# Optimization experiments

Hardware: AMD Instinct MI355X
Metric: run time of the kernel (lower is better)

Reference implementation:

```python
import jax, jax.numpy as jnp
import numpy as np

B, S, D = 4, 2048, 1024
E = 4          # moe_capacity
K = 2          # top-k experts
F = 4 * D      # expert hidden width


def setup_inputs() -> dict:
    key = jax.random.key(0)
    ks = jax.random.split(key, 8)
    scale_in = 1.0 / np.sqrt(D)
    scale_hid = 1.0 / np.sqrt(F)
    return {
        "x": jax.random.normal(ks[0], (B, S, D), dtype=jnp.float32),
        "Wg": jax.random.normal(ks[1], (D, E), dtype=jnp.float32) * scale_in,
        "bg": jnp.zeros((E,), dtype=jnp.float32),
        "W1": jax.random.normal(ks[2], (E, D, F), dtype=jnp.float32) * scale_in,
        "b1": jnp.zeros((E, F), dtype=jnp.float32),
        "W2": jax.random.normal(ks[3], (E, F, D), dtype=jnp.float32) * scale_hid,
        "b2": jnp.zeros((E, D), dtype=jnp.float32),
    }


def reference(x, Wg, bg, W1, b1, W2, b2):
    # Gating: top-k expert indices per token (scores are NOT used as weights
    # in the original module; the combine mask is a binary one-hot sum).
    gate_logits = jnp.einsum("bsd,de->bse", x, Wg) + bg          # [B,S,E]
    _, idx = jax.lax.top_k(gate_logits, K)                        # [B,S,K]
    mask = jnp.sum(jax.nn.one_hot(idx, E, dtype=x.dtype), axis=-2)  # [B,S,E], 0/1

    # All-experts dense compute (faithful to original wasteful fallback).
    h = jax.nn.swish(jnp.einsum("bsd,edf->bsef", x, W1) + b1)     # [B,S,E,F]
    y = jnp.einsum("bsef,efd->bsed", h, W2) + b2                  # [B,S,E,D]

    # Mask-and-sum combine over experts.
    out = jnp.einsum("bsed,bse->bsd", y, mask)                    # [B,S,D]
    return out.astype(jnp.float32)
```

## Files before the change

### kernel.cpp

```cpp
#include <hip/hip_runtime.h>
#include <hip/hip_fp16.h>

#define D_DIM 1024
#define E_NUM 4
#define F_DIM 4096
#define NTOK 8192
#define MT 64
#define FC 256
#define KC 256
#define FHALF 2048
#define NWORK 520
#define NWORK_A 4160
#define NWORK_B 2080
#define HROWS_MAX 16640

typedef _Float16 half8_t __attribute__((ext_vector_type(8)));
typedef _Float16 half4_t __attribute__((ext_vector_type(4)));
typedef float floatx4 __attribute__((ext_vector_type(4)));

template<bool WRITE_XH>
__global__ __launch_bounds__(256) void gate_kernel(
    const float* __restrict__ x, const float* __restrict__ Wg,
    const float* __restrict__ bg, _Float16* __restrict__ xh,
    int* __restrict__ cnt, int* __restrict__ lists)
{
    __shared__ int sel[32];
    __shared__ int loc[4][32];
    __shared__ int lbase[4], lnum[4];

    int wave = threadIdx.x >> 6;
    int lane = threadIdx.x & 63;
    int tbase = blockIdx.x * 32;

    for (int i = 0; i < 8; ++i) {
        int slot = wave * 8 + i;
        int tok = tbase + slot;
        const float* xr = x + (size_t)tok * D_DIM;
        double a0 = 0.0, a1 = 0.0, a2 = 0.0, a3 = 0.0;
        #pragma unroll
        for (int it = 0; it < 4; ++it) {
            int i0 = it * 256 + lane * 4;
            float4 xv = *(const float4*)(xr + i0);
            if (WRITE_XH) {
                half4_t hv = { (_Float16)xv.x, (_Float16)xv.y,
                               (_Float16)xv.z, (_Float16)xv.w };
                *(half4_t*)(xh + (size_t)tok * D_DIM + i0) = hv;
            }
            float4 w0 = *(const float4*)(Wg + (size_t)i0 * 4);
            float4 w1 = *(const float4*)(Wg + (size_t)i0 * 4 + 4);
            float4 w2 = *(const float4*)(Wg + (size_t)i0 * 4 + 8);
            float4 w3 = *(const float4*)(Wg + (size_t)i0 * 4 + 12);
            a0 += (double)xv.x * w0.x + (double)xv.y * w1.x
                + (double)xv.z * w2.x + (double)xv.w * w3.x;
            a1 += (double)xv.x * w0.y + (double)xv.y * w1.y
                + (double)xv.z * w2.y + (double)xv.w * w3.y;
            a2 += (double)xv.x * w0.z + (double)xv.y * w1.z
                + (double)xv.z * w2.z + (double)xv.w * w3.z;
            a3 += (double)xv.x * w0.w + (double)xv.y * w1.w
                + (double)xv.z * w2.w + (double)xv.w * w3.w;
        }
        #pragma unroll
        for (int off = 32; off > 0; off >>= 1) {
            a0 += __shfl_down(a0, off);
            a1 += __shfl_down(a1, off);
            a2 += __shfl_down(a2, off);
            a3 += __shfl_down(a3, off);
        }
        if (lane == 0) {
            double lg[4] = { a0 + (double)bg[0], a1 + (double)bg[1],
                             a2 + (double)bg[2], a3 + (double)bg[3] };
            int i1 = 0;
            for (int e = 1; e < 4; ++e) if (lg[e] > lg[i1]) i1 = e;
            int i2 = -1;
            for (int e = 0; e < 4; ++e) {
                if (e == i1) continue;
                if (i2 < 0 || lg[e] > lg[i2]) i2 = e;
            }
            sel[slot] = i1 * 4 + i2;
        }
    }
    __syncthreads();
    if (threadIdx.x < 4) {
        int e = threadIdx.x, n = 0;
        for (int s = 0; s < 32; ++s) {
            int v = sel[s];
            if ((v >> 2) == e || (v & 3) == e) loc[e][n++] = tbase + s;
        }
        lnum[e] = n;
        lbase[e] = atomicAdd(&cnt[e], n);
    }
    __syncthreads();
    {
        int e = threadIdx.x >> 6;
        int j = threadIdx.x & 63;
        if (j < lnum[e]) lists[e * NTOK + lbase[e] + j] = loc[e][j];
    }
}

__global__ __launch_bounds__(256) void tile_pack_kernel(
    const float* __restrict__ src, _Float16* __restrict__ dst, int R, int C)
{
    __shared__ _Float16 t2[32][36];
    int r0 = blockIdx.y * 32, c0 = blockIdx.x * 32;
    const float* s = src + (size_t)blockIdx.z * R * C;
    _Float16* d = dst + (size_t)blockIdx.z * R * C;
    int tx = threadIdx.x & 31, ty = threadIdx.x >> 5;
    #pragma unroll
    for (int i = 0; i < 4; ++i) {
        int r = ty + i * 8;
        t2[tx][r] = (_Float16)s[(size_t)(r0 + r) * C + c0 + tx];
    }
    __syncthreads();
    int KB = R >> 5;
    int idx = threadIdx.x * 4;
    int frag_h = idx >> 9;
    int rem = idx & 511;
    int quad = rem >> 7, ln = (rem >> 3) & 15, j0 = rem & 7;
    int cl = frag_h * 16 + ln, rl = quad * 8 + j0;
    half4_t v = { t2[cl][rl], t2[cl][rl + 1], t2[cl][rl + 2], t2[cl][rl + 3] };
    size_t off = ((size_t)(((c0 >> 4) + frag_h) * KB + (r0 >> 5))) * 512 + rem;
    *(half4_t*)&d[off] = v;
}

__device__ __forceinline__ void decode_tile(
    int r, int nb0, int nb1, int nb2,
    int& expert, int& tile, int& hbase)
{
    if (r < nb0)                  { expert = 0; tile = r;                 hbase = 0; }
    else if (r < nb0 + nb1)       { expert = 1; tile = r - nb0;           hbase = nb0; }
    else if (r < nb0 + nb1 + nb2) { expert = 2; tile = r - nb0 - nb1;     hbase = nb0 + nb1; }
    else                          { expert = 3; tile = r - nb0 - nb1 - nb2; hbase = nb0 + nb1 + nb2; }
}

__global__ __launch_bounds__(512, 4) void h1_kernel(
    const _Float16* __restrict__ xh, const _Float16* __restrict__ W1m,
    const float* __restrict__ b1, const int* __restrict__ cnt,
    const int* __restrict__ lists, _Float16* __restrict__ Hbuf)
{
    __shared__ _Float16 Xs[MT][KC + 8];
    __shared__ _Float16 Hsd[MT][FC + 8];
    __shared__ int tks[MT];

    int b = blockIdx.x;
    int work = (b & 7) * (NWORK_A / 8) + (b >> 3);

    int nb0 = (cnt[0] + MT - 1) / MT;
    int nb1 = (cnt[1] + MT - 1) / MT;
    int nb2 = (cnt[2] + MT - 1) / MT;
    int nb3 = (cnt[3] + MT - 1) / MT;
    int T = nb0 + nb1 + nb2 + nb3;
    if (work >= 16 * T) return;

    int fc = work / T;
    int r  = work % T;
    int expert, tile, hbase;
    decode_tile(r, nb0, nb1, nb2, expert, tile, hbase);
    int mcnt = min(MT, cnt[expert] - tile * MT);

    if (threadIdx.x < MT) {
        int idx = tile * MT + (int)threadIdx.x;
        tks[threadIdx.x] = lists[expert * NTOK + ((int)threadIdx.x < mcnt ? idx : tile * MT)];
    }
    __syncthreads();

    const half8_t* W1f = (const half8_t*)(W1m + (size_t)expert * D_DIM * F_DIM);
    const float* b1e = b1 + (size_t)expert * F_DIM;

    int w = threadIdx.x >> 6;
    int lane = threadIdx.x & 63;
    int quad = lane >> 4;
    int ln = lane & 15;
    int srow = threadIdx.x >> 3;
    int stg  = threadIdx.x & 7;

    int f0 = fc * FC;
    int fb0 = (f0 >> 4) + w * 2;

    floatx4 hacc[4][2];
    #pragma unroll
    for (int mt = 0; mt < 4; ++mt) { hacc[mt][0] = (floatx4){0.f,0.f,0.f,0.f};
                                     hacc[mt][1] = (floatx4){0.f,0.f,0.f,0.f}; }

    for (int kc = 0; kc < D_DIM / KC; ++kc) {
        int k0 = kc * KC;
        {
            const _Float16* xr = xh + (size_t)tks[srow] * D_DIM + k0 + stg * 32;
            half8_t v0 = *(const half8_t*)(xr);
            half8_t v1 = *(const half8_t*)(xr + 8);
            half8_t v2 = *(const half8_t*)(xr + 16);
            half8_t v3 = *(const half8_t*)(xr + 24);
            *(half8_t*)&Xs[srow][stg * 32]      = v0;
            *(half8_t*)&Xs[srow][stg * 32 + 8]  = v1;
            *(half8_t*)&Xs[srow][stg * 32 + 16] = v2;
            *(half8_t*)&Xs[srow][stg * 32 + 24] = v3;
        }
        __syncthreads();

        #pragma unroll
        for (int ks = 0; ks < KC / 32; ++ks) {
            int kk = ks * 32 + quad * 8;
            int kb = kc * 8 + ks;
            half8_t a[4];
            #pragma unroll
            for (int mt = 0; mt < 4; ++mt)
                a[mt] = *(const half8_t*)&Xs[mt * 16 + ln][kk];
            #pragma unroll
            for (int nt = 0; nt < 2; ++nt) {
                half8_t bfr = W1f[((size_t)((fb0 + nt) * 32 + kb)) * 64 + lane];
                #pragma unroll
                for (int mt = 0; mt < 4; ++mt)
                    hacc[mt][nt] = __builtin_amdgcn_mfma_f32_16x16x32_f16(
                        a[mt], bfr, hacc[mt][nt], 0, 0, 0);
            }
        }
        __syncthreads();
    }

    #pragma unroll
    for (int nt = 0; nt < 2; ++nt) {
        int fcol_l = w * 32 + nt * 16 + ln;
        float b1v = b1e[f0 + fcol_l];
        #pragma unroll
        for (int mt = 0; mt < 4; ++mt)
            #pragma unroll
            for (int r2 = 0; r2 < 4; ++r2) {
                float v = hacc[mt][nt][r2] + b1v;
                float hs = v / (1.f + __expf(-v));
                Hsd[mt * 16 + quad * 4 + r2][fcol_l] = (_Float16)hs;
            }
    }
    __syncthreads();

    {
        size_t hrow0 = ((size_t)(hbase + tile)) * MT;
        _Float16* hdst = Hbuf + (hrow0 + srow) * F_DIM + f0 + stg * 32;
        const _Float16* hsrc = &Hsd[srow][stg * 32];
        half8_t v0 = *(const half8_t*)(hsrc);
        half8_t v1 = *(const half8_t*)(hsrc + 8);
        half8_t v2 = *(const half8_t*)(hsrc + 16);
        half8_t v3 = *(const half8_t*)(hsrc + 24);
        *(half8_t*)(hdst)      = v0;
        *(half8_t*)(hdst + 8)  = v1;
        *(half8_t*)(hdst + 16) = v2;
        *(half8_t*)(hdst + 24) = v3;
    }
}

__global__ __launch_bounds__(512, 4) void o2_kernel(
    const _Float16* __restrict__ Hbuf, const _Float16* __restrict__ W2m,
    const float* __restrict__ b2, const int* __restrict__ cnt,
    const int* __restrict__ lists, float* __restrict__ out)
{
    __shared__ _Float16 Hs[MT][KC + 8];
    __shared__ int tks[MT];

    int b = blockIdx.x;
    int work = (b & 7) * (NWORK_B / 8) + (b >> 3);

    int nb0 = (cnt[0] + MT - 1) / MT;
    int nb1 = (cnt[1] + MT - 1) / MT;
    int nb2 = (cnt[2] + MT - 1) / MT;
    int nb3 = (cnt[3] + MT - 1) / MT;
    int T = nb0 + nb1 + nb2 + nb3;
    if (work >= 8 * T) return;

    int s = work / T;
    int r = work % T;
    int dq = s >> 1;
    int kh = s & 1;
    int expert, tile, hbase;
    decode_tile(r, nb0, nb1, nb2, expert, tile, hbase);
    int mcnt = min(MT, cnt[expert] - tile * MT);

    if (threadIdx.x < MT) {
        int idx = tile * MT + (int)threadIdx.x;
        tks[threadIdx.x] = lists[expert * NTOK + ((int)threadIdx.x < mcnt ? idx : tile * MT)];
    }
    __syncthreads();

    const half8_t* W2f = (const half8_t*)(W2m + (size_t)expert * D_DIM * F_DIM);
    const float* b2e = b2 + (size_t)expert * D_DIM;

    int w = threadIdx.x >> 6;
    int lane = threadIdx.x & 63;
    int quad = lane >> 4;
    int ln = lane & 15;
    int srow = threadIdx.x >> 3;
    int stg  = threadIdx.x & 7;

    size_t hrow0 = ((size_t)(hbase + tile)) * MT;
    const _Float16* hrow = Hbuf + (hrow0 + srow) * F_DIM + stg * 32;

    floatx4 oacc[4][2];
    #pragma unroll
    for (int mt = 0; mt < 4; ++mt) { oacc[mt][0] = (floatx4){0.f,0.f,0.f,0.f};
                                     oacc[mt][1] = (floatx4){0.f,0.f,0.f,0.f}; }

    for (int kc = kh * 8; kc < kh * 8 + 8; ++kc) {
        {
            const _Float16* hr = hrow + kc * KC;
            half8_t v0 = *(const half8_t*)(hr);
            half8_t v1 = *(const half8_t*)(hr + 8);
            half8_t v2 = *(const half8_t*)(hr + 16);
            half8_t v3 = *(const half8_t*)(hr + 24);
            *(half8_t*)&Hs[srow][stg * 32]      = v0;
            *(half8_t*)&Hs[srow][stg * 32 + 8]  = v1;
            *(half8_t*)&Hs[srow][stg * 32 + 16] = v2;
            *(half8_t*)&Hs[srow][stg * 32 + 24] = v3;
        }
        __syncthreads();

        #pragma unroll
        for (int ks = 0; ks < KC / 32; ++ks) {
            int kk = ks * 32 + quad * 8;
            int fkb = kc * 8 + ks;
            half8_t a[4];
            #pragma unroll
            for (int mt = 0; mt < 4; ++mt)
                a[mt] = *(const half8_t*)&Hs[mt * 16 + ln][kk];
            #pragma unroll
            for (int nt = 0; nt < 2; ++nt) {
                int db = dq * 16 + w * 2 + nt;
                half8_t bfr = W2f[((size_t)(db * 128 + fkb)) * 64 + lane];
                #pragma unroll
                for (int mt = 0; mt < 4; ++mt)
                    oacc[mt][nt] = __builtin_amdgcn_mfma_f32_16x16x32_f16(
                        a[mt], bfr, oacc[mt][nt], 0, 0, 0);
            }
        }
        __syncthreads();
    }

    #pragma unroll
    for (int mt = 0; mt < 4; ++mt) {
        #pragma unroll
        for (int r2 = 0; r2 < 4; ++r2) {
            int row = mt * 16 + quad * 4 + r2;
            if (row >= mcnt) continue;
            float* orow = out + (size_t)tks[row] * D_DIM;
            #pragma unroll
            for (int nt = 0; nt < 2; ++nt) {
                int dcol = dq * 256 + w * 32 + nt * 16 + ln;
                float v = oacc[mt][nt][r2];
                if (kh == 0) v += b2e[dcol];
                atomicAdd(orow + dcol, v);
            }
        }
    }
}

__global__ __launch_bounds__(512, 2) void moe_fast_kernel(
    const _Float16* __restrict__ xh, const _Float16* __restrict__ W1m,
    const float* __restrict__ b1, const _Float16* __restrict__ W2m,
    const float* __restrict__ b2, const int* __restrict__ cnt,
    const int* __restrict__ lists, float* __restrict__ out)
{
    __shared__ _Float16 Xs[MT][KC + 8];
    __shared__ _Float16 Hsd[MT][FC + 8];
    __shared__ int tks[MT];

    int b = blockIdx.x;
    int work = (b & 7) * (NWORK / 8) + (b >> 3);

    int nb0 = (cnt[0] + MT - 1) / MT;
    int nb1 = (cnt[1] + MT - 1) / MT;
    int nb2 = (cnt[2] + MT - 1) / MT;
    int nb3 = (cnt[3] + MT - 1) / MT;
    int T = nb0 + nb1 + nb2 + nb3;

    int fhalf, r;
    if (work < T) { fhalf = 0; r = work; }
    else if (work < 2 * T) { fhalf = 1; r = work - T; }
    else return;

    int expert, tile, hbase;
    decode_tile(r, nb0, nb1, nb2, expert, tile, hbase);
    int mcnt = min(MT, cnt[expert] - tile * MT);

    if (threadIdx.x < MT) {
        int idx = tile * MT + (int)threadIdx.x;
        tks[threadIdx.x] = lists[expert * NTOK + ((int)threadIdx.x < mcnt ? idx : tile * MT)];
    }
    __syncthreads();

    const half8_t* W1f = (const half8_t*)(W1m + (size_t)expert * D_DIM * F_DIM);
    const half8_t* W2f = (const half8_t*)(W2m + (size_t)expert * D_DIM * F_DIM);
    const float* b1e = b1 + (size_t)expert * F_DIM;
    const float* b2e = b2 + (size_t)expert * D_DIM;

    int w = threadIdx.x >> 6;
    int lane = threadIdx.x & 63;
    int quad = lane >> 4;
    int ln = lane & 15;

    floatx4 oacc[4][8];
    #pragma unroll
    for (int mt = 0; mt < 4; ++mt)
        #pragma unroll
        for (int nt = 0; nt < 8; ++nt)
            oacc[mt][nt] = (floatx4){0.f, 0.f, 0.f, 0.f};

    int fbase = fhalf * FHALF;
    int srow = threadIdx.x >> 3;
    int stg  = threadIdx.x & 7;

    for (int fc = 0; fc < FHALF / FC; ++fc) {
        int f0 = fbase + fc * FC;
        int fb0 = (f0 >> 4) + w * 2;

        floatx4 hacc[4][2];
        #pragma unroll
        for (int mt = 0; mt < 4; ++mt) { hacc[mt][0] = (floatx4){0.f,0.f,0.f,0.f};
                                         hacc[mt][1] = (floatx4){0.f,0.f,0.f,0.f}; }

        for (int kc = 0; kc < D_DIM / KC; ++kc) {
            int k0 = kc * KC;
            {
                const _Float16* xr = xh + (size_t)tks[srow] * D_DIM + k0 + stg * 32;
                half8_t v0 = *(const half8_t*)(xr);
                half8_t v1 = *(const half8_t*)(xr + 8);
                half8_t v2 = *(const half8_t*)(xr + 16);
                half8_t v3 = *(const half8_t*)(xr + 24);
                *(half8_t*)&Xs[srow][stg * 32]      = v0;
                *(half8_t*)&Xs[srow][stg * 32 + 8]  = v1;
                *(half8_t*)&Xs[srow][stg * 32 + 16] = v2;
                *(half8_t*)&Xs[srow][stg * 32 + 24] = v3;
            }
            __syncthreads();

            #pragma unroll
            for (int ks = 0; ks < KC / 32; ++ks) {
                int kk = ks * 32 + quad * 8;
                int kb = kc * 8 + ks;
                half8_t a[4];
                #pragma unroll
                for (int mt = 0; mt < 4; ++mt)
                    a[mt] = *(const half8_t*)&Xs[mt * 16 + ln][kk];
                #pragma unroll
                for (int nt = 0; nt < 2; ++nt) {
                    half8_t bfr = W1f[((size_t)((fb0 + nt) * 32 + kb)) * 64 + lane];
                    #pragma unroll
                    for (int mt = 0; mt < 4; ++mt)
                        hacc[mt][nt] = __builtin_amdgcn_mfma_f32_16x16x32_f16(
                            a[mt], bfr, hacc[mt][nt], 0, 0, 0);
                }
            }
            __syncthreads();
        }

        #pragma unroll
        for (int nt = 0; nt < 2; ++nt) {
            int fcol_l = w * 32 + nt * 16 + ln;
            float b1v = b1e[f0 + fcol_l];
            #pragma unroll
            for (int mt = 0; mt < 4; ++mt)
                #pragma unroll
                for (int r2 = 0; r2 < 4; ++r2) {
                    float v = hacc[mt][nt][r2] + b1v;
                    float hs = v / (1.f + __expf(-v));
                    Hsd[mt * 16 + quad * 4 + r2][fcol_l] = (_Float16)hs;
                }
        }
        __syncthreads();

        #pragma unroll
        for (int ks = 0; ks < FC / 32; ++ks) {
            int kk = ks * 32 + quad * 8;
            int fkb = (f0 >> 5) + ks;
            half8_t a[4];
            #pragma unroll
            for (int mt = 0; mt < 4; ++mt)
                a[mt] = *(const half8_t*)&Hsd[mt * 16 + ln][kk];
            #pragma unroll
            for (int nt = 0; nt < 8; ++nt) {
                int db = w * 8 + nt;
                half8_t bfr = W2f[((size_t)(db * 128 + fkb)) * 64 + lane];
                #pragma unroll
                for (int mt = 0; mt < 4; ++mt)
                    oacc[mt][nt] = __builtin_amdgcn_mfma_f32_16x16x32_f16(
                        a[mt], bfr, oacc[mt][nt], 0, 0, 0);
            }
        }
        __syncthreads();
    }

    #pragma unroll
    for (int mt = 0; mt < 4; ++mt) {
        #pragma unroll
        for (int r2 = 0; r2 < 4; ++r2) {
            int row = mt * 16 + quad * 4 + r2;
            if (row >= mcnt) continue;
            float* orow = out + (size_t)tks[row] * D_DIM;
            #pragma unroll
            for (int nt = 0; nt < 8; ++nt) {
                int dcol = w * 128 + nt * 16 + ln;
                float v = oacc[mt][nt][r2];
                if (fhalf == 0) v += b2e[dcol];
                atomicAdd(orow + dcol, v);
            }
        }
    }
}

__global__ __launch_bounds__(512, 2) void moe_slow_kernel(
    const float* __restrict__ x, const float* __restrict__ W1,
    const float* __restrict__ b1, const float* __restrict__ W2,
    const float* __restrict__ b2, const int* __restrict__ cnt,
    const int* __restrict__ lists, float* __restrict__ out)
{
    __shared__ _Float16 Xs[MT][KC + 8];
    __shared__ _Float16 Hsd[MT][FC + 8];
    __shared__ int tks[MT];

    int fhalf = blockIdx.x & 1;
    int bi = blockIdx.x >> 1;
    int expert = -1, tile = 0, mcnt = 0;
    int rem = bi;
    for (int e = 0; e < E_NUM; ++e) {
        int n = cnt[e];
        int nbt = (n + MT - 1) / MT;
        if (rem < nbt) { expert = e; tile = rem; mcnt = min(MT, n - rem * MT); break; }
        rem -= nbt;
    }
    if (expert < 0) return;

    if (threadIdx.x < MT) {
        int idx = tile * MT + (int)threadIdx.x;
        tks[threadIdx.x] = lists[expert * NTOK + ((int)threadIdx.x < mcnt ? idx : tile * MT)];
    }
    __syncthreads();

    const float* W1e = W1 + (size_t)expert * D_DIM * F_DIM;
    const float* W2e = W2 + (size_t)expert * F_DIM * D_DIM;
    const float* b1e = b1 + (size_t)expert * F_DIM;
    const float* b2e = b2 + (size_t)expert * D_DIM;

    int w = threadIdx.x >> 6;
    int lane = threadIdx.x & 63;
    int quad = lane >> 4;
    int ln = lane & 15;

    floatx4 oacc[4][8];
    #pragma unroll
    for (int mt = 0; mt < 4; ++mt)
        #pragma unroll
        for (int nt = 0; nt < 8; ++nt)
            oacc[mt][nt] = (floatx4){0.f, 0.f, 0.f, 0.f};

    int fbase = fhalf * FHALF;
    int srow = threadIdx.x >> 3;
    int stg  = threadIdx.x & 7;

    for (int fc = 0; fc < FHALF / FC; ++fc) {
        int f0 = fbase + fc * FC;
        floatx4 hacc[4][2];
        #pragma unroll
        for (int mt = 0; mt < 4; ++mt) { hacc[mt][0] = (floatx4){0.f,0.f,0.f,0.f};
                                         hacc[mt][1] = (floatx4){0.f,0.f,0.f,0.f}; }
        for (int kc = 0; kc < D_DIM / KC; ++kc) {
            int k0 = kc * KC;
            {
                const float* xr = x + (size_t)tks[srow] * D_DIM + k0;
                #pragma unroll
                for (int j = 0; j < 8; ++j) {
                    int c = (stg + j * 8) * 4;
                    float4 v = *(const float4*)(xr + c);
                    half4_t hv = { (_Float16)v.x, (_Float16)v.y,
                                   (_Float16)v.z, (_Float16)v.w };
                    *(half4_t*)&Xs[srow][c] = hv;
                }
            }
            __syncthreads();
            #pragma unroll
            for (int ks = 0; ks < KC / 32; ++ks) {
                int kk = ks * 32 + quad * 8;
                half8_t a[4];
                #pragma unroll
                for (int mt = 0; mt < 4; ++mt)
                    a[mt] = *(const half8_t*)&Xs[mt * 16 + ln][kk];
                #pragma unroll
                for (int nt = 0; nt < 2; ++nt) {
                    int fcol = f0 + w * 32 + nt * 16 + ln;
                    const float* wp = W1e + (size_t)(k0 + kk) * F_DIM + fcol;
                    half8_t bfr;
                    #pragma unroll
                    for (int j = 0; j < 8; ++j)
                        bfr[j] = (_Float16)wp[(size_t)j * F_DIM];
                    #pragma unroll
                    for (int mt = 0; mt < 4; ++mt)
                        hacc[mt][nt] = __builtin_amdgcn_mfma_f32_16x16x32_f16(
                            a[mt], bfr, hacc[mt][nt], 0, 0, 0);
                }
            }
            __syncthreads();
        }
        #pragma unroll
        for (int nt = 0; nt < 2; ++nt) {
            int fcol_l = w * 32 + nt * 16 + ln;
            float b1v = b1e[f0 + fcol_l];
            #pragma unroll
            for (int mt = 0; mt < 4; ++mt)
                #pragma unroll
                for (int r2 = 0; r2 < 4; ++r2) {
                    float v = hacc[mt][nt][r2] + b1v;
                    float hs = v / (1.f + __expf(-v));
                    Hsd[mt * 16 + quad * 4 + r2][fcol_l] = (_Float16)hs;
                }
        }
        __syncthreads();
        #pragma unroll
        for (int ks = 0; ks < FC / 32; ++ks) {
            int kk = ks * 32 + quad * 8;
            half8_t a[4];
            #pragma unroll
            for (int mt = 0; mt < 4; ++mt)
                a[mt] = *(const half8_t*)&Hsd[mt * 16 + ln][kk];
            #pragma unroll
            for (int nt = 0; nt < 8; ++nt) {
                int dcol = w * 128 + nt * 16 + ln;
                const float* wp = W2e + (size_t)(f0 + kk) * D_DIM + dcol;
                half8_t bfr;
                #pragma unroll
                for (int j = 0; j < 8; ++j)
                    bfr[j] = (_Float16)wp[(size_t)j * D_DIM];
                #pragma unroll
                for (int mt = 0; mt < 4; ++mt)
                    oacc[mt][nt] = __builtin_amdgcn_mfma_f32_16x16x32_f16(
                        a[mt], bfr, oacc[mt][nt], 0, 0, 0);
            }
        }
        __syncthreads();
    }
    #pragma unroll
    for (int mt = 0; mt < 4; ++mt) {
        #pragma unroll
        for (int r2 = 0; r2 < 4; ++r2) {
            int row = mt * 16 + quad * 4 + r2;
            if (row >= mcnt) continue;
            float* orow = out + (size_t)tks[row] * D_DIM;
            #pragma unroll
            for (int nt = 0; nt < 8; ++nt) {
                int dcol = w * 128 + nt * 16 + ln;
                float v = oacc[mt][nt][r2];
                if (fhalf == 0) v += b2e[dcol];
                atomicAdd(orow + dcol, v);
            }
        }
    }
}

extern "C" void kernel_launch(void* const* d_in, const int* in_sizes, int n_in,
                              void* d_out, int out_size, void* d_ws, size_t ws_size,
                              hipStream_t stream) {
    const float* x  = (const float*)d_in[0];
    const float* Wg = (const float*)d_in[1];
    const float* bg = (const float*)d_in[2];
    const float* W1 = (const float*)d_in[3];
    const float* b1 = (const float*)d_in[4];
    const float* W2 = (const float*)d_in[5];
    const float* b2 = (const float*)d_in[6];
    float* out = (float*)d_out;

    const size_t OFF_LISTS = 512;
    const size_t OFF_W1M   = 131584;
    const size_t OFF_W2M   = OFF_W1M + (size_t)E_NUM * D_DIM * F_DIM * 2;
    const size_t OFF_XH    = OFF_W2M + (size_t)E_NUM * D_DIM * F_DIM * 2;
    const size_t OFF_H     = OFF_XH + (size_t)NTOK * D_DIM * 2;
    const size_t WS_NEED   = OFF_H;
    const size_t WS_NEED2  = OFF_H + (size_t)HROWS_MAX * F_DIM * 2;

    int* cnt   = (int*)d_ws;
    int* lists = (int*)((char*)d_ws + OFF_LISTS);

    hipMemsetAsync(cnt, 0, 16, stream);
    hipMemsetAsync(d_out, 0, (size_t)out_size * sizeof(float), stream);

    if (ws_size >= WS_NEED) {
        _Float16* W1m = (_Float16*)((char*)d_ws + OFF_W1M);
        _Float16* W2m = (_Float16*)((char*)d_ws + OFF_W2M);
        _Float16* xh  = (_Float16*)((char*)d_ws + OFF_XH);

        gate_kernel<true><<<NTOK / 32, 256, 0, stream>>>(x, Wg, bg, xh, cnt, lists);

        tile_pack_kernel<<<dim3(F_DIM / 32, D_DIM / 32, E_NUM), 256, 0, stream>>>(
            W1, W1m, D_DIM, F_DIM);
        tile_pack_kernel<<<dim3(D_DIM / 32, F_DIM / 32, E_NUM), 256, 0, stream>>>(
            W2, W2m, F_DIM, D_DIM);

        if (ws_size >= WS_NEED2) {
            _Float16* Hbuf = (_Float16*)((char*)d_ws + OFF_H);
            h1_kernel<<<NWORK_A, 512, 0, stream>>>(xh, W1m, b1, cnt, lists, Hbuf);
            o2_kernel<<<NWORK_B, 512, 0, stream>>>(Hbuf, W2m, b2, cnt, lists, out);
        } else {
            moe_fast_kernel<<<NWORK, 512, 0, stream>>>(xh, W1m, b1, W2m, b2, cnt, lists, out);
        }
    } else {
        gate_kernel<false><<<NTOK / 32, 256, 0, stream>>>(x, Wg, bg, nullptr, cnt, lists);
        moe_slow_kernel<<<520, 512, 0, stream>>>(x, W1, b1, W2, b2, cnt, lists, out);
    }
}
```

Measured before the change: 672.5 us.

## Double per-block output tiles in MoE GEMMs and widen weight pack tiles

The h1 kernel now computes 512 hidden columns per block instead of 256, reusing each staged X tile across two F sub-tiles. The o2 kernel covers 512 output columns per block instead of 256, reusing each staged H tile across four N fragments. Block counts are halved to match. The weight pack kernel handles 64-column tiles and writes 8-half vectors per thread. Together these cut redundant activation loads and gathers per MFMA, at the cost of more accumulator registers and fewer blocks in flight.

```diff
diff --git a/kernel.cpp b/kernel.cpp
--- a/kernel.cpp
+++ b/kernel.cpp
@@ -10,8 +10,8 @@
 #define KC 256
 #define FHALF 2048
 #define NWORK 520
-#define NWORK_A 4160
-#define NWORK_B 2080
+#define NWORK_A 2080
+#define NWORK_B 1040
 #define HROWS_MAX 16640
 
 typedef _Float16 half8_t __attribute__((ext_vector_type(8)));
@@ -100,26 +100,28 @@
 __global__ __launch_bounds__(256) void tile_pack_kernel(
     const float* __restrict__ src, _Float16* __restrict__ dst, int R, int C)
 {
-    __shared__ _Float16 t2[32][36];
-    int r0 = blockIdx.y * 32, c0 = blockIdx.x * 32;
+    __shared__ _Float16 t2[64][36];
+    int r0 = blockIdx.y * 32, c0 = blockIdx.x * 64;
     const float* s = src + (size_t)blockIdx.z * R * C;
     _Float16* d = dst + (size_t)blockIdx.z * R * C;
-    int tx = threadIdx.x & 31, ty = threadIdx.x >> 5;
-    #pragma unroll
-    for (int i = 0; i < 4; ++i) {
-        int r = ty + i * 8;
+    int tx = threadIdx.x & 63, ty = threadIdx.x >> 6;
+    #pragma unroll
+    for (int i = 0; i < 8; ++i) {
+        int r = ty + i * 4;
         t2[tx][r] = (_Float16)s[(size_t)(r0 + r) * C + c0 + tx];
     }
     __syncthreads();
     int KB = R >> 5;
-    int idx = threadIdx.x * 4;
-    int frag_h = idx >> 9;
-    int rem = idx & 511;
-    int quad = rem >> 7, ln = (rem >> 3) & 15, j0 = rem & 7;
-    int cl = frag_h * 16 + ln, rl = quad * 8 + j0;
-    half4_t v = { t2[cl][rl], t2[cl][rl + 1], t2[cl][rl + 2], t2[cl][rl + 3] };
-    size_t off = ((size_t)(((c0 >> 4) + frag_h) * KB + (r0 >> 5))) * 512 + rem;
-    *(half4_t*)&d[off] = v;
+    int nb_l = threadIdx.x >> 6;
+    int tt = threadIdx.x & 63;
+    int quad = tt >> 4, ln = tt & 15;
+    half8_t v;
+    #pragma unroll
+    for (int j = 0; j < 8; ++j)
+        v[j] = t2[nb_l * 16 + ln][quad * 8 + j];
+    size_t off = ((size_t)((c0 >> 4) + nb_l) * KB + (r0 >> 5)) * 512
+               + quad * 128 + ln * 8;
+    *(half8_t*)&d[off] = v;
 }
 
 __device__ __forceinline__ void decode_tile(
@@ -149,9 +151,9 @@
     int nb2 = (cnt[2] + MT - 1) / MT;
     int nb3 = (cnt[3] + MT - 1) / MT;
     int T = nb0 + nb1 + nb2 + nb3;
-    if (work >= 16 * T) return;
-
-    int fc = work / T;
+    if (work >= 8 * T) return;
+
+    int fc2 = work / T;
     int r  = work % T;
     int expert, tile, hbase;
     decode_tile(r, nb0, nb1, nb2, expert, tile, hbase);
@@ -173,13 +175,16 @@
     int srow = threadIdx.x >> 3;
     int stg  = threadIdx.x & 7;
 
-    int f0 = fc * FC;
-    int fb0 = (f0 >> 4) + w * 2;
-
-    floatx4 hacc[4][2];
-    #pragma unroll
-    for (int mt = 0; mt < 4; ++mt) { hacc[mt][0] = (floatx4){0.f,0.f,0.f,0.f};
-                                     hacc[mt][1] = (floatx4){0.f,0.f,0.f,0.f}; }
+    int f0 = fc2 * 512;
+
+    floatx4 hacc[2][4][2];
+    #pragma unroll
+    for (int fh = 0; fh < 2; ++fh)
+        #pragma unroll
+        for (int mt = 0; mt < 4; ++mt) {
+            hacc[fh][mt][0] = (floatx4){0.f,0.f,0.f,0.f};
+            hacc[fh][mt][1] = (floatx4){0.f,0.f,0.f,0.f};
+        }
 
     for (int kc = 0; kc < D_DIM / KC; ++kc) {
         int k0 = kc * KC;
@@ -205,44 +210,52 @@
             for (int mt = 0; mt < 4; ++mt)
                 a[mt] = *(const half8_t*)&Xs[mt * 16 + ln][kk];
             #pragma unroll
-            for (int nt = 0; nt < 2; ++nt) {
-                half8_t bfr = W1f[((size_t)((fb0 + nt) * 32 + kb)) * 64 + lane];
-                #pragma unroll
-                for (int mt = 0; mt < 4; ++mt)
-                    hacc[mt][nt] = __builtin_amdgcn_mfma_f32_16x16x32_f16(
-                        a[mt], bfr, hacc[mt][nt], 0, 0, 0);
-            }
-        }
-        __syncthreads();
-    }
-
-    #pragma unroll
-    for (int nt = 0; nt < 2; ++nt) {
-        int fcol_l = w * 32 + nt * 16 + ln;
-        float b1v = b1e[f0 + fcol_l];
-        #pragma unroll
-        for (int mt = 0; mt < 4; ++mt)
-            #pragma unroll
-            for (int r2 = 0; r2 < 4; ++r2) {
-                float v = hacc[mt][nt][r2] + b1v;
-                float hs = v / (1.f + __expf(-v));
-                Hsd[mt * 16 + quad * 4 + r2][fcol_l] = (_Float16)hs;
-            }
-    }
-    __syncthreads();
-
-    {
-        size_t hrow0 = ((size_t)(hbase + tile)) * MT;
-        _Float16* hdst = Hbuf + (hrow0 + srow) * F_DIM + f0 + stg * 32;
-        const _Float16* hsrc = &Hsd[srow][stg * 32];
-        half8_t v0 = *(const half8_t*)(hsrc);
-        half8_t v1 = *(const half8_t*)(hsrc + 8);
-        half8_t v2 = *(const half8_t*)(hsrc + 16);
-        half8_t v3 = *(const half8_t*)(hsrc + 24);
-        *(half8_t*)(hdst)      = v0;
-        *(half8_t*)(hdst + 8)  = v1;
-        *(half8_t*)(hdst + 16) = v2;
-        *(half8_t*)(hdst + 24) = v3;
+            for (int fh = 0; fh < 2; ++fh) {
+                int fb0 = ((f0 + fh * 256) >> 4) + w * 2;
+                #pragma unroll
+                for (int nt = 0; nt < 2; ++nt) {
+                    half8_t bfr = W1f[((size_t)((fb0 + nt) * 32 + kb)) * 64 + lane];
+                    #pragma unroll
+                    for (int mt = 0; mt < 4; ++mt)
+                        hacc[fh][mt][nt] = __builtin_amdgcn_mfma_f32_16x16x32_f16(
+                            a[mt], bfr, hacc[fh][mt][nt], 0, 0, 0);
+                }
+            }
+        }
+        __syncthreads();
+    }
+
+    size_t hrow0 = ((size_t)(hbase + tile)) * MT;
+    #pragma unroll
+    for (int fh = 0; fh < 2; ++fh) {
+        int fbase = f0 + fh * 256;
+        #pragma unroll
+        for (int nt = 0; nt < 2; ++nt) {
+            int fcol_l = w * 32 + nt * 16 + ln;
+            float b1v = b1e[fbase + fcol_l];
+            #pragma unroll
+            for (int mt = 0; mt < 4; ++mt)
+                #pragma unroll
+                for (int r2 = 0; r2 < 4; ++r2) {
+                    float v = hacc[fh][mt][nt][r2] + b1v;
+                    float hs = v / (1.f + __expf(-v));
+                    Hsd[mt * 16 + quad * 4 + r2][fcol_l] = (_Float16)hs;
+                }
+        }
+        __syncthreads();
+        {
+            _Float16* hdst = Hbuf + (hrow0 + srow) * F_DIM + fbase + stg * 32;
+            const _Float16* hsrc = &Hsd[srow][stg * 32];
+            half8_t v0 = *(const half8_t*)(hsrc);
+            half8_t v1 = *(const half8_t*)(hsrc + 8);
+            half8_t v2 = *(const half8_t*)(hsrc + 16);
+            half8_t v3 = *(const half8_t*)(hsrc + 24);
+            *(half8_t*)(hdst)      = v0;
+            *(half8_t*)(hdst + 8)  = v1;
+            *(half8_t*)(hdst + 16) = v2;
+            *(half8_t*)(hdst + 24) = v3;
+        }
+        __syncthreads();
     }
 }
 
@@ -262,11 +275,11 @@
     int nb2 = (cnt[2] + MT - 1) / MT;
     int nb3 = (cnt[3] + MT - 1) / MT;
     int T = nb0 + nb1 + nb2 + nb3;
-    if (work >= 8 * T) return;
+    if (work >= 4 * T) return;
 
     int s = work / T;
     int r = work % T;
-    int dq = s >> 1;
+    int dh = s >> 1;
     int kh = s & 1;
     int expert, tile, hbase;
     decode_tile(r, nb0, nb1, nb2, expert, tile, hbase);
@@ -291,10 +304,12 @@
     size_t hrow0 = ((size_t)(hbase + tile)) * MT;
     const _Float16* hrow = Hbuf + (hrow0 + srow) * F_DIM + stg * 32;
 
-    floatx4 oacc[4][2];
-    #pragma unroll
-    for (int mt = 0; mt < 4; ++mt) { oacc[mt][0] = (floatx4){0.f,0.f,0.f,0.f};
-                                     oacc[mt][1] = (floatx4){0.f,0.f,0.f,0.f}; }
+    floatx4 oacc[4][4];
+    #pragma unroll
+    for (int mt = 0; mt < 4; ++mt)
+        #pragma unroll
+        for (int nt = 0; nt < 4; ++nt)
+            oacc[mt][nt] = (floatx4){0.f,0.f,0.f,0.f};
 
     for (int kc = kh * 8; kc < kh * 8 + 8; ++kc) {
         {
@@ -319,8 +334,8 @@
             for (int mt = 0; mt < 4; ++mt)
                 a[mt] = *(const half8_t*)&Hs[mt * 16 + ln][kk];
             #pragma unroll
-            for (int nt = 0; nt < 2; ++nt) {
-                int db = dq * 16 + w * 2 + nt;
+            for (int nt = 0; nt < 4; ++nt) {
+                int db = dh * 32 + w * 4 + nt;
                 half8_t bfr = W2f[((size_t)(db * 128 + fkb)) * 64 + lane];
                 #pragma unroll
                 for (int mt = 0; mt < 4; ++mt)
@@ -339,8 +354,8 @@
             if (row >= mcnt) continue;
             float* orow = out + (size_t)tks[row] * D_DIM;
             #pragma unroll
-            for (int nt = 0; nt < 2; ++nt) {
-                int dcol = dq * 256 + w * 32 + nt * 16 + ln;
+            for (int nt = 0; nt < 4; ++nt) {
+                int dcol = dh * 512 + w * 64 + nt * 16 + ln;
                 float v = oacc[mt][nt][r2];
                 if (kh == 0) v += b2e[dcol];
                 atomicAdd(orow + dcol, v);
@@ -682,9 +697,9 @@
 
         gate_kernel<true><<<NTOK / 32, 256, 0, stream>>>(x, Wg, bg, xh, cnt, lists);
 
-        tile_pack_kernel<<<dim3(F_DIM / 32, D_DIM / 32, E_NUM), 256, 0, stream>>>(
+        tile_pack_kernel<<<dim3(F_DIM / 64, D_DIM / 32, E_NUM), 256, 0, stream>>>(
             W1, W1m, D_DIM, F_DIM);
-        tile_pack_kernel<<<dim3(D_DIM / 32, F_DIM / 32, E_NUM), 256, 0, stream>>>(
+        tile_pack_kernel<<<dim3(D_DIM / 64, F_DIM / 32, E_NUM), 256, 0, stream>>>(
             W2, W2m, F_DIM, D_DIM);
 
         if (ws_size >= WS_NEED2) {
```

Measured after the change: 875.4 us. +30.2%, slower.
